# Kernel tuning notes

Hardware: AMD Instinct MI355X
Metric: run time of the kernel (lower is better)

## Reference

```python
import jax, jax.numpy as jnp
import numpy as np

H = 8          # num_heads
D = 256        # num_hiddens (left == right embed dim)
DH = D // H    # per-head dim
SH = 64        # num_attention_score_hiddens
B = 4
L_LEFT = 128
L_RIGHT = 256
NEG = -1e6


def _split_heads(x):
    # [B, L, D] -> [B*H, L, D/H]
    b, l, d = x.shape
    return x.reshape(b, l, H, d // H).transpose(0, 2, 1, 3).reshape(b * H, l, d // H)


def _merge_heads(x):
    # [B*H, L, dh] -> [B, L, H*dh]
    bh, l, dh = x.shape
    return x.reshape(-1, H, l, dh).transpose(0, 2, 1, 3).reshape(-1, l, H * dh)


def _additive_attention(q, k, v, valid, Wq, Wk, wv):
    # q: [BH, Lq, dh], k/v: [BH, Lk, dh], valid: [BH] int
    qf = q @ Wq                                   # [BH, Lq, SH]
    kf = k @ Wk                                   # [BH, Lk, SH]
    feats = jnp.tanh(qf[:, :, None, :] + kf[:, None, :, :])   # [BH, Lq, Lk, SH]
    scores = jnp.einsum('bqkh,h->bqk', feats, wv)              # [BH, Lq, Lk]
    lk = k.shape[1]
    mask = jnp.arange(lk)[None, None, :] < valid[:, None, None]
    scores = jnp.where(mask, scores, NEG)
    w = jax.nn.softmax(scores, axis=-1)
    return w @ v                                  # [BH, Lq, dh]


def setup_inputs() -> dict:
    key = jax.random.key(0)
    ks = jax.random.split(key, 16)
    f32 = jnp.float32
    s_w = 1.0 / np.sqrt(DH)
    s_v = 1.0 / np.sqrt(SH)
    s_o = 1.0 / np.sqrt(D)
    return {
        'queries_left': jax.random.normal(ks[0], (B, L_LEFT, D), f32),
        'keys_right':   jax.random.normal(ks[1], (B, L_RIGHT, D), f32),
        'values_right': jax.random.normal(ks[2], (B, L_RIGHT, D), f32),
        'queries_right': jax.random.normal(ks[3], (B, L_RIGHT, D), f32),
        'keys_left':    jax.random.normal(ks[4], (B, L_LEFT, D), f32),
        'values_left':  jax.random.normal(ks[5], (B, L_LEFT, D), f32),
        'Wq_l': jax.random.normal(ks[6], (DH, SH), f32) * s_w,
        'Wk_l': jax.random.normal(ks[7], (DH, SH), f32) * s_w,
        'wv_l': jax.random.normal(ks[8], (SH,), f32) * s_v,
        'Wo_l': jax.random.normal(ks[9], (D, D), f32) * s_o,
        'Wq_r': jax.random.normal(ks[10], (DH, SH), f32) * s_w,
        'Wk_r': jax.random.normal(ks[11], (DH, SH), f32) * s_w,
        'wv_r': jax.random.normal(ks[12], (SH,), f32) * s_v,
        'Wo_r': jax.random.normal(ks[13], (D, D), f32) * s_o,
        'valid_lens_right': jax.random.randint(ks[14], (B,), 1, L_RIGHT + 1).astype(jnp.int32),
        'valid_lens_left':  jax.random.randint(ks[15], (B,), 1, L_LEFT + 1).astype(jnp.int32),
    }


def reference(queries_left, keys_right, values_right, queries_right, keys_left,
              values_left, Wq_l, Wk_l, wv_l, Wo_l, Wq_r, Wk_r, wv_r, Wo_r,
              valid_lens_right, valid_lens_left):
    ql = _split_heads(queries_left)
    kr = _split_heads(keys_right)
    vr = _split_heads(values_right)
    qr = _split_heads(queries_right)
    kl = _split_heads(keys_left)
    vl = _split_heads(values_left)
    vlr = jnp.repeat(valid_lens_right, H)   # [B*H]
    vll = jnp.repeat(valid_lens_left, H)
    out_l = _additive_attention(ql, kr, vr, vlr, Wq_l, Wk_l, wv_l)
    out_r = _additive_attention(qr, kl, vl, vll, Wq_r, Wk_r, wv_r)
    out_l = _merge_heads(out_l) @ Wo_l      # [B, L_LEFT, D]
    out_r = _merge_heads(out_r) @ Wo_r      # [B, L_RIGHT, D]
    return out_l, out_r
```

## Files before the change

kernel.cpp:

```cpp
#include <hip/hip_runtime.h>
#include <math.h>


#define LOG2E 1.4426950408889634f
#define SCALE2 (2.0f * LOG2E)
#define NEGS  (-2.0f * LOG2E)

#define OFF_EQL 0
#define OFF_EKL 262144
#define OFF_EQR 786432
#define OFF_EKR 1310720
#define OFF_HOL 1572864
#define OFF_HOR 1703936

static __device__ __forceinline__ float fast_exp2(float x) {
#if __has_builtin(__builtin_amdgcn_exp2f)
    return __builtin_amdgcn_exp2f(x);
#else
    return exp2f(x);
#endif
}
static __device__ __forceinline__ float fast_rcp(float x) {
#if __has_builtin(__builtin_amdgcn_rcpf)
    return __builtin_amdgcn_rcpf(x);
#else
    return 1.0f / x;
#endif
}

__global__ __launch_bounds__(256) void k1_proj(
    const float* __restrict__ ql, const float* __restrict__ kr,
    const float* __restrict__ qr, const float* __restrict__ kl,
    const float* __restrict__ wql, const float* __restrict__ wkl,
    const float* __restrict__ wqr, const float* __restrict__ wkr,
    float* __restrict__ ws)
{
    __shared__ float tlds[64 * 17];
    int blk = blockIdx.x;
    const float* X; const float* W; float* out; int L; int ktype;
    if (blk < 256)       { X = ql; W = wql; out = ws + OFF_EQL; L = 128; ktype = 0; }
    else if (blk < 768)  { X = kr; W = wkl; out = ws + OFF_EKL; L = 256; ktype = 1; blk -= 256; }
    else if (blk < 1280) { X = qr; W = wqr; out = ws + OFF_EQR; L = 256; ktype = 0; blk -= 768; }
    else                 { X = kl; W = wkr; out = ws + OFF_EKR; L = 128; ktype = 1; blk -= 1280; }

    const int tiles = L >> 4;
    const int bh = blk / tiles;
    const int l0 = (blk - bh * tiles) << 4;
    const int b = bh >> 3, hd = bh & 7;
    const int t = threadIdx.x;
    const int h = t & 63, lsub = t >> 6;

    float wcol[32];
#pragma unroll
    for (int j = 0; j < 32; ++j) wcol[j] = W[j * 64 + h];

    const float* xb = X + ((b * L + l0 + lsub * 4) * 256) + hd * 32;

#pragma unroll
    for (int i = 0; i < 4; ++i) {
        const float4* xp = (const float4*)(xb + i * 256);
        float acc = 0.f;
#pragma unroll
        for (int j4 = 0; j4 < 8; ++j4) {
            float4 a = xp[j4];
            acc += a.x * wcol[4 * j4 + 0];
            acc += a.y * wcol[4 * j4 + 1];
            acc += a.z * wcol[4 * j4 + 2];
            acc += a.w * wcol[4 * j4 + 3];
        }
        const float e = fast_exp2(acc * SCALE2);
        const int lloc = lsub * 4 + i;
        if (!ktype) out[(bh * L + l0 + lloc) * 64 + h] = e;
        else        tlds[h * 17 + lloc] = e;
    }
    if (ktype) {
        __syncthreads();
        const int ll = t & 15, hq = t >> 4;
#pragma unroll
        for (int hh = 0; hh < 4; ++hh) {
            const int h2 = hq + 16 * hh;
            out[bh * (64 * L) + h2 * L + l0 + ll] = tlds[h2 * 17 + ll];
        }
    }
}

template<int LK, int LQ, int TQ>
static __device__ __forceinline__ void attn_fused(
    int bh, int q0,
    const float* __restrict__ eq, const float* __restrict__ ek,
    const float* __restrict__ wv, const float* __restrict__ v,
    int valid, float* __restrict__ ho,
    float* P_lds, float* pv_lds)
{
    constexpr int RPT = TQ / 4;
    constexpr int J   = LK / 64;
    constexpr int CS  = LK / 8;
    const int t = threadIdx.x;
    const int lane = t & 63, w = t >> 6;
    const int b = bh >> 3, hd = bh & 7;

    {
        const int row0 = w * RPT;
        float acc[RPT][J];
#pragma unroll
        for (int r = 0; r < RPT; ++r)
#pragma unroll
            for (int j = 0; j < J; ++j) acc[r][j] = 0.f;

        const float* ekb = ek + bh * (64 * LK) + lane;
        const float* eqb = eq + (bh * LQ + q0 + row0) * 64;

#pragma unroll
        for (int j = 0; j < J; ++j) {
            if (64 * j < valid) {
#pragma unroll
                for (int hc = 0; hc < 16; ++hc) {
                    const float4 wv4 = *(const float4*)(wv + hc * 4);
                    float wva[4] = {wv4.x, wv4.y, wv4.z, wv4.w};
                    float eqa[RPT][4];
#pragma unroll
                    for (int r = 0; r < RPT; ++r) {
                        const float4 q4 = *(const float4*)(eqb + r * 64 + hc * 4);
                        eqa[r][0] = q4.x; eqa[r][1] = q4.y;
                        eqa[r][2] = q4.z; eqa[r][3] = q4.w;
                    }
#pragma unroll
                    for (int hs = 0; hs < 4; ++hs) {
                        const float ekv = ekb[(hc * 4 + hs) * LK + 64 * j];
#pragma unroll
                        for (int pr = 0; pr < RPT / 2; ++pr) {
                            const float d0 = fmaf(eqa[2 * pr    ][hs], ekv, 1.0f);
                            const float d1 = fmaf(eqa[2 * pr + 1][hs], ekv, 1.0f);
                            const float rr = fast_rcp(d0 * d1);
                            acc[2 * pr    ][j] += (wva[hs] * d1) * rr;
                            acc[2 * pr + 1][j] += (wva[hs] * d0) * rr;
                        }
                    }
                }
            }
        }

#pragma unroll
        for (int r = 0; r < RPT; ++r) {
            float sv[J];
            float m = -3.0e38f;
#pragma unroll
            for (int j = 0; j < J; ++j) {
                sv[j] = (64 * j + lane < valid) ? acc[r][j] * NEGS : -1.0e6f;
                m = fmaxf(m, sv[j]);
            }
#pragma unroll
            for (int off = 1; off < 64; off <<= 1) m = fmaxf(m, __shfl_xor(m, off));
            float lsum = 0.f;
#pragma unroll
            for (int j = 0; j < J; ++j) { sv[j] = fast_exp2(sv[j] - m); lsum += sv[j]; }
#pragma unroll
            for (int off = 1; off < 64; off <<= 1) lsum += __shfl_xor(lsum, off);
            const float inv = fast_rcp(lsum);
#pragma unroll
            for (int j = 0; j < J; ++j)
                P_lds[(row0 + r) * LK + 64 * j + lane] = sv[j] * inv;
        }
    }
    __syncthreads();

    {
        const int d = t & 31, kc = t >> 5;
        float acc2[TQ];
#pragma unroll
        for (int row = 0; row < TQ; ++row) acc2[row] = 0.f;

        if (kc * CS < valid) {
            const float* vp = v + (b * LK + kc * CS) * 256 + hd * 32 + d;
#pragma unroll
            for (int c = 0; c < CS / 8; ++c) {
                float vv[8];
#pragma unroll
                for (int i = 0; i < 8; ++i) vv[i] = vp[(c * 8 + i) * 256];
#pragma unroll
                for (int row = 0; row < TQ; ++row) {
                    const float4* pp = (const float4*)(P_lds + row * LK + kc * CS + c * 8);
                    const float4 p0 = pp[0], p1 = pp[1];
                    acc2[row] += p0.x * vv[0] + p0.y * vv[1] + p0.z * vv[2] + p0.w * vv[3]
                               + p1.x * vv[4] + p1.y * vv[5] + p1.z * vv[6] + p1.w * vv[7];
                }
            }
        }
#pragma unroll
        for (int row = 0; row < TQ; ++row)
            pv_lds[(kc * TQ + row) * 32 + d] = acc2[row];
    }
    __syncthreads();

#pragma unroll
    for (int rr = 0; rr < (TQ * 32) / 256; ++rr) {
        const int idx = t + 256 * rr;
        const int dd = idx & 31, row = idx >> 5;
        float o = 0.f;
#pragma unroll
        for (int kc2 = 0; kc2 < 8; ++kc2) o += pv_lds[(kc2 * TQ + row) * 32 + dd];
        ho[(b * LQ + q0 + row) * 256 + hd * 32 + dd] = o;
    }
}

__global__ __launch_bounds__(256, 6) void k2_attn(
    const float* __restrict__ eql, const float* __restrict__ ekl,
    const float* __restrict__ eqr, const float* __restrict__ ekr,
    const float* __restrict__ wvl, const float* __restrict__ wvr,
    const float* __restrict__ vr, const float* __restrict__ vl,
    const int* __restrict__ vlr, const int* __restrict__ vll,
    float* __restrict__ hol, float* __restrict__ hor)
{
    __shared__ __align__(16) float P_lds[2048];
    __shared__ __align__(16) float pv_lds[4096];
    int blk = blockIdx.x;
    if (blk < 512) {
        const int bh = blk >> 4, q0 = (blk & 15) << 3;
        attn_fused<256, 128, 8>(bh, q0, eql, ekl, wvl, vr, vlr[bh >> 3],
                                hol, P_lds, pv_lds);
    } else {
        blk -= 512;
        const int bh = blk >> 4, q0 = (blk & 15) << 4;
        attn_fused<128, 256, 16>(bh, q0, eqr, ekr, wvr, vl, vll[bh >> 3],
                                 hor, P_lds, pv_lds);
    }
}

__global__ __launch_bounds__(256) void k3_proj(
    const float* __restrict__ ws,
    const float* __restrict__ wol, const float* __restrict__ wor,
    float* __restrict__ out)
{
    __shared__ __align__(16) float a_lds[1024];
    const int row0 = blockIdx.x * 4;
    const float* A; const float* W; float* op; int lr0;
    if (row0 < 512) { A = ws + OFF_HOL; W = wol; op = out;          lr0 = row0; }
    else            { A = ws + OFF_HOR; W = wor; op = out + 131072; lr0 = row0 - 512; }

    const int t = threadIdx.x;
#pragma unroll
    for (int i = 0; i < 4; ++i) a_lds[i * 256 + t] = A[(lr0 + i) * 256 + t];
    __syncthreads();

    float acc[4];
#pragma unroll
    for (int r = 0; r < 4; ++r) acc[r] = 0.f;

#pragma unroll 4
    for (int k4 = 0; k4 < 64; ++k4) {
        const float w0 = W[(k4 * 4 + 0) * 256 + t];
        const float w1 = W[(k4 * 4 + 1) * 256 + t];
        const float w2 = W[(k4 * 4 + 2) * 256 + t];
        const float w3 = W[(k4 * 4 + 3) * 256 + t];
#pragma unroll
        for (int r = 0; r < 4; ++r) {
            const float4 a = *(const float4*)(a_lds + r * 256 + k4 * 4);
            acc[r] += a.x * w0 + a.y * w1 + a.z * w2 + a.w * w3;
        }
    }
#pragma unroll
    for (int r = 0; r < 4; ++r) op[(lr0 + r) * 256 + t] = acc[r];
}

extern "C" void kernel_launch(void* const* d_in, const int* in_sizes, int n_in,
                              void* d_out, int out_size, void* d_ws, size_t ws_size,
                              hipStream_t stream)
{
    const float* ql  = (const float*)d_in[0];
    const float* kr  = (const float*)d_in[1];
    const float* vr  = (const float*)d_in[2];
    const float* qr  = (const float*)d_in[3];
    const float* kl  = (const float*)d_in[4];
    const float* vl  = (const float*)d_in[5];
    const float* wql = (const float*)d_in[6];
    const float* wkl = (const float*)d_in[7];
    const float* wvl = (const float*)d_in[8];
    const float* wol = (const float*)d_in[9];
    const float* wqr = (const float*)d_in[10];
    const float* wkr = (const float*)d_in[11];
    const float* wvr = (const float*)d_in[12];
    const float* wor = (const float*)d_in[13];
    const int*   vlr = (const int*)d_in[14];
    const int*   vll = (const int*)d_in[15];
    float* ws  = (float*)d_ws;
    float* out = (float*)d_out;

    hipLaunchKernelGGL(k1_proj, dim3(1536), dim3(256), 0, stream,
                       ql, kr, qr, kl, wql, wkl, wqr, wkr, ws);
    hipLaunchKernelGGL(k2_attn, dim3(1024), dim3(256), 0, stream,
                       ws + OFF_EQL, ws + OFF_EKL, ws + OFF_EQR, ws + OFF_EKR,
                       wvl, wvr, vr, vl, vlr, vll,
                       ws + OFF_HOL, ws + OFF_HOR);
    hipLaunchKernelGGL(k3_proj, dim3(384), dim3(256), 0, stream,
                       ws, wol, wor, out);
}
```

Measured before the change: 131.9 us.

## Fuse query projection into attention kernel and pair tanh terms differently

The query projection (x·Wq followed by exp) now runs inside the attention kernel, with results kept in LDS, so k1 only projects keys. This drops the global write and re-read of the projected queries and halves k1's grid. The inner score loop also switches to pairing two feature dimensions per reciprocal instead of two query rows, using fma accumulation. In exchange the attention blocks do redundant projection work per query tile, add a barrier, and use more LDS, which may lower occupancy.

```diff
diff --git a/kernel.cpp b/kernel.cpp
--- a/kernel.cpp
+++ b/kernel.cpp
@@ -6,12 +6,10 @@
 #define SCALE2 (2.0f * LOG2E)
 #define NEGS  (-2.0f * LOG2E)
 
-#define OFF_EQL 0
-#define OFF_EKL 262144
-#define OFF_EQR 786432
-#define OFF_EKR 1310720
-#define OFF_HOL 1572864
-#define OFF_HOR 1703936
+#define OFF_EKL 0
+#define OFF_EKR 524288
+#define OFF_HOL 786432
+#define OFF_HOR 917504
 
 static __device__ __forceinline__ float fast_exp2(float x) {
 #if __has_builtin(__builtin_amdgcn_exp2f)
@@ -29,19 +27,15 @@
 }
 
 __global__ __launch_bounds__(256) void k1_proj(
-    const float* __restrict__ ql, const float* __restrict__ kr,
-    const float* __restrict__ qr, const float* __restrict__ kl,
-    const float* __restrict__ wql, const float* __restrict__ wkl,
-    const float* __restrict__ wqr, const float* __restrict__ wkr,
+    const float* __restrict__ kr, const float* __restrict__ kl,
+    const float* __restrict__ wkl, const float* __restrict__ wkr,
     float* __restrict__ ws)
 {
     __shared__ float tlds[64 * 17];
     int blk = blockIdx.x;
-    const float* X; const float* W; float* out; int L; int ktype;
-    if (blk < 256)       { X = ql; W = wql; out = ws + OFF_EQL; L = 128; ktype = 0; }
-    else if (blk < 768)  { X = kr; W = wkl; out = ws + OFF_EKL; L = 256; ktype = 1; blk -= 256; }
-    else if (blk < 1280) { X = qr; W = wqr; out = ws + OFF_EQR; L = 256; ktype = 0; blk -= 768; }
-    else                 { X = kl; W = wkr; out = ws + OFF_EKR; L = 128; ktype = 1; blk -= 1280; }
+    const float* X; const float* W; float* out; int L;
+    if (blk < 512) { X = kr; W = wkl; out = ws + OFF_EKL; L = 256; }
+    else           { X = kl; W = wkr; out = ws + OFF_EKR; L = 128; blk -= 512; }
 
     const int tiles = L >> 4;
     const int bh = blk / tiles;
@@ -68,29 +62,25 @@
             acc += a.z * wcol[4 * j4 + 2];
             acc += a.w * wcol[4 * j4 + 3];
         }
-        const float e = fast_exp2(acc * SCALE2);
-        const int lloc = lsub * 4 + i;
-        if (!ktype) out[(bh * L + l0 + lloc) * 64 + h] = e;
-        else        tlds[h * 17 + lloc] = e;
-    }
-    if (ktype) {
-        __syncthreads();
-        const int ll = t & 15, hq = t >> 4;
-#pragma unroll
-        for (int hh = 0; hh < 4; ++hh) {
-            const int h2 = hq + 16 * hh;
-            out[bh * (64 * L) + h2 * L + l0 + ll] = tlds[h2 * 17 + ll];
-        }
+        tlds[h * 17 + lsub * 4 + i] = fast_exp2(acc * SCALE2);
+    }
+    __syncthreads();
+    const int ll = t & 15, hq = t >> 4;
+#pragma unroll
+    for (int hh = 0; hh < 4; ++hh) {
+        const int h2 = hq + 16 * hh;
+        out[bh * (64 * L) + h2 * L + l0 + ll] = tlds[h2 * 17 + ll];
     }
 }
 
 template<int LK, int LQ, int TQ>
 static __device__ __forceinline__ void attn_fused(
     int bh, int q0,
-    const float* __restrict__ eq, const float* __restrict__ ek,
+    const float* __restrict__ xq, const float* __restrict__ wq,
+    const float* __restrict__ ek,
     const float* __restrict__ wv, const float* __restrict__ v,
     int valid, float* __restrict__ ho,
-    float* P_lds, float* pv_lds)
+    float* P_lds, float* pv_lds, float* eq_lds)
 {
     constexpr int RPT = TQ / 4;
     constexpr int J   = LK / 64;
@@ -100,6 +90,29 @@
     const int b = bh >> 3, hd = bh & 7;
 
     {
+        const int h = lane;
+        float wcol[32];
+#pragma unroll
+        for (int j = 0; j < 32; ++j) wcol[j] = wq[j * 64 + h];
+#pragma unroll
+        for (int i = 0; i < TQ / 4; ++i) {
+            const int r = w + 4 * i;
+            const float4* xp = (const float4*)(xq + (b * LQ + q0 + r) * 256 + hd * 32);
+            float acc = 0.f;
+#pragma unroll
+            for (int j4 = 0; j4 < 8; ++j4) {
+                float4 a = xp[j4];
+                acc += a.x * wcol[4 * j4 + 0];
+                acc += a.y * wcol[4 * j4 + 1];
+                acc += a.z * wcol[4 * j4 + 2];
+                acc += a.w * wcol[4 * j4 + 3];
+            }
+            eq_lds[r * 64 + h] = fast_exp2(acc * SCALE2);
+        }
+    }
+    __syncthreads();
+
+    {
         const int row0 = w * RPT;
         float acc[RPT][J];
 #pragma unroll
@@ -108,7 +121,6 @@
             for (int j = 0; j < J; ++j) acc[r][j] = 0.f;
 
         const float* ekb = ek + bh * (64 * LK) + lane;
-        const float* eqb = eq + (bh * LQ + q0 + row0) * 64;
 
 #pragma unroll
         for (int j = 0; j < J; ++j) {
@@ -120,20 +132,21 @@
                     float eqa[RPT][4];
 #pragma unroll
                     for (int r = 0; r < RPT; ++r) {
-                        const float4 q4 = *(const float4*)(eqb + r * 64 + hc * 4);
+                        const float4 q4 = *(const float4*)(eq_lds + (row0 + r) * 64 + hc * 4);
                         eqa[r][0] = q4.x; eqa[r][1] = q4.y;
                         eqa[r][2] = q4.z; eqa[r][3] = q4.w;
                     }
 #pragma unroll
-                    for (int hs = 0; hs < 4; ++hs) {
-                        const float ekv = ekb[(hc * 4 + hs) * LK + 64 * j];
-#pragma unroll
-                        for (int pr = 0; pr < RPT / 2; ++pr) {
-                            const float d0 = fmaf(eqa[2 * pr    ][hs], ekv, 1.0f);
-                            const float d1 = fmaf(eqa[2 * pr + 1][hs], ekv, 1.0f);
-                            const float rr = fast_rcp(d0 * d1);
-                            acc[2 * pr    ][j] += (wva[hs] * d1) * rr;
-                            acc[2 * pr + 1][j] += (wva[hs] * d0) * rr;
+                    for (int hp = 0; hp < 2; ++hp) {
+                        const float ek0 = ekb[(hc * 4 + 2 * hp    ) * LK + 64 * j];
+                        const float ek1 = ekb[(hc * 4 + 2 * hp + 1) * LK + 64 * j];
+#pragma unroll
+                        for (int r = 0; r < RPT; ++r) {
+                            const float da = fmaf(eqa[r][2 * hp    ], ek0, 1.0f);
+                            const float db = fmaf(eqa[r][2 * hp + 1], ek1, 1.0f);
+                            float n = wva[2 * hp] * db;
+                            n = fmaf(wva[2 * hp + 1], da, n);
+                            acc[r][j] = fmaf(n, fast_rcp(da * db), acc[r][j]);
                         }
                     }
                 }
@@ -204,8 +217,9 @@
 }
 
 __global__ __launch_bounds__(256, 6) void k2_attn(
-    const float* __restrict__ eql, const float* __restrict__ ekl,
-    const float* __restrict__ eqr, const float* __restrict__ ekr,
+    const float* __restrict__ ql, const float* __restrict__ qr,
+    const float* __restrict__ wql, const float* __restrict__ wqr,
+    const float* __restrict__ ekl, const float* __restrict__ ekr,
     const float* __restrict__ wvl, const float* __restrict__ wvr,
     const float* __restrict__ vr, const float* __restrict__ vl,
     const int* __restrict__ vlr, const int* __restrict__ vll,
@@ -213,16 +227,17 @@
 {
     __shared__ __align__(16) float P_lds[2048];
     __shared__ __align__(16) float pv_lds[4096];
+    __shared__ __align__(16) float eq_lds[1024];
     int blk = blockIdx.x;
     if (blk < 512) {
         const int bh = blk >> 4, q0 = (blk & 15) << 3;
-        attn_fused<256, 128, 8>(bh, q0, eql, ekl, wvl, vr, vlr[bh >> 3],
-                                hol, P_lds, pv_lds);
+        attn_fused<256, 128, 8>(bh, q0, ql, wql, ekl, wvl, vr, vlr[bh >> 3],
+                                hol, P_lds, pv_lds, eq_lds);
     } else {
         blk -= 512;
         const int bh = blk >> 4, q0 = (blk & 15) << 4;
-        attn_fused<128, 256, 16>(bh, q0, eqr, ekr, wvr, vl, vll[bh >> 3],
-                                 hor, P_lds, pv_lds);
+        attn_fused<128, 256, 16>(bh, q0, qr, wqr, ekr, wvr, vl, vll[bh >> 3],
+                                 hor, P_lds, pv_lds, eq_lds);
     }
 }
 
@@ -285,10 +300,10 @@
     float* ws  = (float*)d_ws;
     float* out = (float*)d_out;
 
-    hipLaunchKernelGGL(k1_proj, dim3(1536), dim3(256), 0, stream,
-                       ql, kr, qr, kl, wql, wkl, wqr, wkr, ws);
+    hipLaunchKernelGGL(k1_proj, dim3(768), dim3(256), 0, stream,
+                       kr, kl, wkl, wkr, ws);
     hipLaunchKernelGGL(k2_attn, dim3(1024), dim3(256), 0, stream,
-                       ws + OFF_EQL, ws + OFF_EKL, ws + OFF_EQR, ws + OFF_EKR,
+                       ql, qr, wql, wqr, ws + OFF_EKL, ws + OFF_EKR,
                        wvl, wvr, vr, vl, vlr, vll,
                        ws + OFF_HOL, ws + OFF_HOR);
     hipLaunchKernelGGL(k3_proj, dim3(384), dim3(256), 0, stream,
```

New measurement: 120.7 us (median of 2 runs). -8.5%, faster.
